# Kernel tuning notes

Measured on AMD Instinct MI355X. Metric: run time of the kernel, lower is better.

## Reference

```python
import jax, jax.numpy as jnp
import numpy as np

N_HEADS = 16


def _apply_rope(x, rope):
    # x: [B, H, N, Dh], rope: [B, N, Dh]; consecutive (even, odd) pairs form complex numbers
    xr, xi = x[..., 0::2], x[..., 1::2]              # [B,H,N,Dh/2]
    rr, ri = rope[:, None, :, 0::2], rope[:, None, :, 1::2]  # [B,1,N,Dh/2]
    or_ = xr * rr - xi * ri
    oi = xr * ri + xi * rr
    return jnp.stack([or_, oi], axis=-1).reshape(x.shape)


def setup_inputs() -> dict:
    key = jax.random.key(0)
    ks = jax.random.split(key, 8)
    B, N, D, Dh = 2, 2048, 2048, 128
    s = 0.02
    return {
        "x": jax.random.normal(ks[0], (B, N, D), jnp.float32),
        "q_rope": jax.random.normal(ks[1], (B, N, Dh), jnp.float32),
        "k_rope": jax.random.normal(ks[2], (B, N, Dh), jnp.float32),
        "Wq": jax.random.normal(ks[3], (D, D), jnp.float32) * s,
        "Wk": jax.random.normal(ks[4], (D, D), jnp.float32) * s,
        "Wv": jax.random.normal(ks[5], (D, D), jnp.float32) * s,
        "Wo": jax.random.normal(ks[6], (D, D), jnp.float32) * s,
        "bo": jax.random.normal(ks[7], (D,), jnp.float32) * s,
    }


def reference(x, q_rope, k_rope, Wq, Wk, Wv, Wo, bo):
    B, N, D = x.shape
    H = N_HEADS
    Dh = D // H
    # QKV projections (weights stored as [in, out])
    q = (x @ Wq).reshape(B, N, H, Dh).transpose(0, 2, 1, 3)  # [B,H,N,Dh]
    k = (x @ Wk).reshape(B, N, H, Dh).transpose(0, 2, 1, 3)
    v = (x @ Wv).reshape(B, N, H, Dh).transpose(0, 2, 1, 3)
    # NOTE: original scales q by d_head^-0.5 AND F.sdpa applies its default
    # 1/sqrt(d_head) scale again -> total score scale 1/d_head (faithful).
    q = q * (Dh ** -0.5)
    q = _apply_rope(q, q_rope)
    k = _apply_rope(k, k_rope)
    scores = jnp.einsum('bhnd,bhmd->bhnm', q, k) * (Dh ** -0.5)
    attn = jax.nn.softmax(scores, axis=-1)
    out = jnp.einsum('bhnm,bhmd->bhnd', attn, v)  # [B,H,N,Dh]
    out = out.transpose(0, 2, 1, 3).reshape(B, N, D)
    return out @ Wo + bo
```

## Files before the change

### kernel.cpp

```cpp
#include <hip/hip_runtime.h>
#include <hip/hip_bf16.h>
#include <stdint.h>


typedef __attribute__((ext_vector_type(4))) float f32x4;
typedef __attribute__((ext_vector_type(8))) short bf16x8;

__device__ __forceinline__ unsigned short f2bf(float f){
  unsigned u = __builtin_bit_cast(unsigned, f);
  u += 0x7FFFu + ((u >> 16) & 1u);
  return (unsigned short)(u >> 16);
}
__device__ __forceinline__ float bf2f(unsigned short h){
  unsigned u = ((unsigned)h) << 16;
  return __builtin_bit_cast(float, u);
}
__device__ __forceinline__ void gload16(const void* g, void* l){
  __builtin_amdgcn_global_load_lds((const __attribute__((address_space(1))) void*)g,
                                   (__attribute__((address_space(3))) void*)l, 16, 0, 0);
}
__device__ __forceinline__ void drain_all(){
  asm volatile("s_waitcnt vmcnt(0) lgkmcnt(0)" ::: "memory");
  __builtin_amdgcn_sched_barrier(0);
}

__global__ void k_cvt(const float* __restrict__ src, unsigned short* __restrict__ dst, int n4){
  int i = blockIdx.x * 256 + threadIdx.x;
  if (i >= n4) return;
  float4 v = ((const float4*)src)[i];
  unsigned long long pk = (unsigned long long)f2bf(v.x)
    | ((unsigned long long)f2bf(v.y) << 16)
    | ((unsigned long long)f2bf(v.z) << 32)
    | ((unsigned long long)f2bf(v.w) << 48);
  ((unsigned long long*)dst)[i] = pk;
}

__global__ void k_transpose_all(const float* __restrict__ W0, const float* __restrict__ W1,
                                const float* __restrict__ W2, const float* __restrict__ W3,
                                unsigned short* __restrict__ WT){
  const float* W = (blockIdx.z == 0) ? W0 : (blockIdx.z == 1) ? W1 : (blockIdx.z == 2) ? W2 : W3;
  unsigned short* dst = WT + (size_t)blockIdx.z * 4194304;
  __shared__ float tile[64][65];
  int t = threadIdx.x;
  int cc = t & 63, rb = t >> 6;
  int bx = blockIdx.x * 64;
  int by = blockIdx.y * 64;
  #pragma unroll
  for (int i = 0; i < 16; i++){
    int r = rb + i * 4;
    tile[r][cc] = W[(size_t)(by + r) * 2048 + bx + cc];
  }
  __syncthreads();
  #pragma unroll
  for (int i = 0; i < 16; i++){
    int r = rb + i * 4;
    dst[(size_t)(bx + r) * 2048 + by + cc] = f2bf(tile[cc][r]);
  }
}

__global__ __launch_bounds__(512, 2) void k_gemm_qkv(
    const unsigned short* __restrict__ A,
    const unsigned short* __restrict__ Bt,
    unsigned short* __restrict__ Oq,
    unsigned short* __restrict__ Ok,
    unsigned short* __restrict__ Ov,
    const float* __restrict__ ropeq,
    const float* __restrict__ ropek)
{
  const int Kdim = 2048;
  __shared__ char sh[98304];
  const int tid = threadIdx.x;
  const int w = tid >> 6, l = tid & 63, g = l >> 4, c = l & 15;
  const int i0 = blockIdx.y * 16 + blockIdx.x;
  const int xcd = i0 & 7, r0 = i0 >> 3;
  const int bm = (xcd * 2 + (r0 & 1)) * 256;
  const int bn = (r0 >> 1) * 128;
  const int mw = (w >> 1) * 64, nw = (w & 1) * 64;
  f32x4 acc[4][4] = {};
  const int srow = l >> 3;
  const int sbyte = (((l & 7) ^ srow) << 4);
  const char* Ab = (const char*)A;
  const char* Bb = (const char*)Bt;

  auto stage = [&](int kt, int buf){
    char* Abuf = sh + buf * 49152;
    char* Bbuf = Abuf + 32768;
    #pragma unroll
    for (int j = 0; j < 4; j++){
      int ch = w * 4 + j;
      int row = ch * 8 + srow;
      gload16(Ab + ((size_t)(bm + row) * Kdim + kt) * 2 + sbyte, Abuf + ch * 1024);
    }
    #pragma unroll
    for (int j = 0; j < 2; j++){
      int ch = w * 2 + j;
      int row = ch * 8 + srow;
      gload16(Bb + ((size_t)(bn + row) * Kdim + kt) * 2 + sbyte, Bbuf + ch * 1024);
    }
  };

  stage(0, 0);
  drain_all();
  __syncthreads();
  for (int t = 0; t < 32; t++){
    int cur = t & 1;
    if (t < 31) stage((t + 1) * 64, cur ^ 1);
    char* Abuf = sh + cur * 49152;
    char* Bbuf = Abuf + 32768;
    #pragma unroll
    for (int kk = 0; kk < 2; kk++){
      bf16x8 av[4], bv[4];
      #pragma unroll
      for (int i = 0; i < 4; i++){
        int m = mw + i * 16 + c;
        av[i] = *(const bf16x8*)(Abuf + m * 128 + ((kk * 64 + g * 16) ^ ((m & 7) << 4)));
        int n = nw + i * 16 + c;
        bv[i] = *(const bf16x8*)(Bbuf + n * 128 + ((kk * 64 + g * 16) ^ ((n & 7) << 4)));
      }
      #pragma unroll
      for (int i = 0; i < 4; i++)
        #pragma unroll
        for (int jj = 0; jj < 4; jj++)
          acc[i][jj] = __builtin_amdgcn_mfma_f32_16x16x32_bf16(av[i], bv[jj], acc[i][jj], 0, 0, 0);
    }
    drain_all();
    __syncthreads();
  }

  const int matsel = bn >> 11;
  const int hh = (bn >> 7) & 15;
  if (matsel < 2){
    unsigned short* O = matsel ? Ok : Oq;
    const float* rope = matsel ? ropek : ropeq;
    const float scale = matsel ? 1.0f : (1.0f / 128.0f);
    #pragma unroll
    for (int i = 0; i < 4; i++){
      int m0 = bm + mw + i * 16 + g * 4;
      #pragma unroll
      for (int jj = 0; jj < 4; jj++){
        int d = nw + jj * 16 + c;
        int dbase = d & ~1;
        int odd = d & 1;
        #pragma unroll
        for (int r = 0; r < 4; r++){
          int m = m0 + r;
          int b = m >> 11, tok = m & 2047;
          float v = acc[i][jj][r];
          float vp = __shfl_xor(v, 1);
          float2 rv = *(const float2*)(rope + (((size_t)(b * 2048 + tok)) << 7) + dbase);
          float xr = odd ? vp : v;
          float xi = odd ? v : vp;
          float res = odd ? (xr * rv.y + xi * rv.x) : (xr * rv.x - xi * rv.y);
          O[(((size_t)(b * 16 + hh) * 2048 + tok) << 7) + d] = f2bf(res * scale);
        }
      }
    }
  } else {
    #pragma unroll
    for (int i = 0; i < 4; i++){
      int m0 = bm + mw + i * 16 + g * 4;
      int b = m0 >> 11, tok0 = m0 & 2047;
      #pragma unroll
      for (int jj = 0; jj < 4; jj++){
        int d = nw + jj * 16 + c;
        unsigned long long pk = (unsigned long long)f2bf(acc[i][jj][0])
          | ((unsigned long long)f2bf(acc[i][jj][1]) << 16)
          | ((unsigned long long)f2bf(acc[i][jj][2]) << 32)
          | ((unsigned long long)f2bf(acc[i][jj][3]) << 48);
        *(unsigned long long*)(Ov + ((size_t)(b * 16 + hh) * 128 + d) * 2048 + tok0) = pk;
      }
    }
  }
}

__global__ __launch_bounds__(512, 2) void k_gemm_out(
    const unsigned short* __restrict__ A,
    const unsigned short* __restrict__ Bt,
    float* __restrict__ O,
    const float* __restrict__ bias)
{
  const int Kdim = 2048;
  __shared__ char sh[98304];
  const int tid = threadIdx.x;
  const int w = tid >> 6, l = tid & 63, g = l >> 4, c = l & 15;
  const int i0 = blockIdx.y * 16 + blockIdx.x;
  const int xcd = i0 & 7, r0 = i0 >> 3;
  const int bm = (xcd * 2 + (r0 & 1)) * 256;
  const int bn = (r0 >> 1) * 128;
  const int mw = (w >> 1) * 64, nw = (w & 1) * 64;
  f32x4 acc[4][4] = {};
  const int srow = l >> 3;
  const int sbyte = (((l & 7) ^ srow) << 4);
  const char* Ab = (const char*)A;
  const char* Bb = (const char*)Bt;

  auto stage = [&](int kt, int buf){
    char* Abuf = sh + buf * 49152;
    char* Bbuf = Abuf + 32768;
    #pragma unroll
    for (int j = 0; j < 4; j++){
      int ch = w * 4 + j;
      int row = ch * 8 + srow;
      gload16(Ab + ((size_t)(bm + row) * Kdim + kt) * 2 + sbyte, Abuf + ch * 1024);
    }
    #pragma unroll
    for (int j = 0; j < 2; j++){
      int ch = w * 2 + j;
      int row = ch * 8 + srow;
      gload16(Bb + ((size_t)(bn + row) * Kdim + kt) * 2 + sbyte, Bbuf + ch * 1024);
    }
  };

  stage(0, 0);
  drain_all();
  __syncthreads();
  for (int t = 0; t < 32; t++){
    int cur = t & 1;
    if (t < 31) stage((t + 1) * 64, cur ^ 1);
    char* Abuf = sh + cur * 49152;
    char* Bbuf = Abuf + 32768;
    #pragma unroll
    for (int kk = 0; kk < 2; kk++){
      bf16x8 av[4], bv[4];
      #pragma unroll
      for (int i = 0; i < 4; i++){
        int m = mw + i * 16 + c;
        av[i] = *(const bf16x8*)(Abuf + m * 128 + ((kk * 64 + g * 16) ^ ((m & 7) << 4)));
        int n = nw + i * 16 + c;
        bv[i] = *(const bf16x8*)(Bbuf + n * 128 + ((kk * 64 + g * 16) ^ ((n & 7) << 4)));
      }
      #pragma unroll
      for (int i = 0; i < 4; i++)
        #pragma unroll
        for (int jj = 0; jj < 4; jj++)
          acc[i][jj] = __builtin_amdgcn_mfma_f32_16x16x32_bf16(av[i], bv[jj], acc[i][jj], 0, 0, 0);
    }
    drain_all();
    __syncthreads();
  }
  #pragma unroll
  for (int i = 0; i < 4; i++){
    int m0 = bm + mw + i * 16 + g * 4;
    #pragma unroll
    for (int jj = 0; jj < 4; jj++){
      int n = bn + nw + jj * 16 + c;
      float bv2 = bias[n];
      #pragma unroll
      for (int r = 0; r < 4; r++)
        O[(size_t)(m0 + r) * 2048 + n] = acc[i][jj][r] + bv2;
    }
  }
}

__global__ __launch_bounds__(256, 2) void k_attn(
    const unsigned short* __restrict__ Q,
    const unsigned short* __restrict__ Kg,
    const unsigned short* __restrict__ VT,
    unsigned short* __restrict__ Ao)
{
  __shared__ char sh[81920];
  char* PsB = sh + 65536;
  const int tid = threadIdx.x;
  const int w = tid >> 6, l = tid & 63, g = l >> 4, c = l & 15;
  const int i0 = blockIdx.y * 16 + blockIdx.x;
  const int xcd = i0 & 7, kb2 = i0 >> 3;
  const int bh = xcd * 4 + (kb2 >> 4);
  const int qt = kb2 & 15;
  const char* Qb = (const char*)(Q + (((size_t)bh * 2048 + qt * 128) << 7));
  const char* Kb = (const char*)(Kg + ((size_t)bh << 18));
  const char* Vb = (const char*)(VT + ((size_t)bh << 18));
  const int rsub = l >> 4;
  const int byte0 = (l & 15) << 4;
  const int drow = l >> 3;
  const int vbyte = (((l & 7) ^ drow) << 4);

  #pragma unroll
  for (int j = 0; j < 8; j++){
    int chunk = w * 8 + j;
    int row = chunk * 4 + rsub;
    gload16(Qb + (size_t)row * 256 + (byte0 ^ ((row & 7) << 4)), sh + chunk * 1024);
  }
  __syncthreads();
  bf16x8 qa[4][2];
  #pragma unroll
  for (int kk = 0; kk < 4; kk++)
    #pragma unroll
    for (int mf = 0; mf < 2; mf++){
      int q = w * 32 + mf * 16 + c;
      qa[kk][mf] = *(const bf16x8*)(sh + q * 256 + ((kk * 64 + g * 16) ^ ((q & 7) << 4)));
    }
  __syncthreads();

  auto stageKV = [&](int kv, int buf){
    char* Kc = sh + buf * 16384;
    char* Vc = sh + 32768 + buf * 16384;
    #pragma unroll
    for (int j = 0; j < 4; j++){
      int chunk = w * 4 + j;
      int row = chunk * 4 + rsub;
      gload16(Kb + (size_t)(kv * 64 + row) * 256 + (byte0 ^ ((row & 7) << 4)), Kc + chunk * 1024);
    }
    #pragma unroll
    for (int j = 0; j < 4; j++){
      int chunk = w * 4 + j;
      int d = chunk * 8 + drow;
      gload16(Vb + (size_t)d * 4096 + kv * 128 + vbyte, Vc + chunk * 1024);
    }
  };

  f32x4 oacc[2][8] = {};
  float lpart[2][4] = {};

  stageKV(0, 0);
  __syncthreads();

  for (int kv = 0; kv < 32; kv++){
    int cur = kv & 1;
    if (kv < 31) stageKV(kv + 1, cur ^ 1);
    char* Kc = sh + cur * 16384;
    char* Vc = sh + 32768 + cur * 16384;

    f32x4 sacc[2][4] = {};
    __builtin_amdgcn_s_setprio(1);
    #pragma unroll
    for (int kk = 0; kk < 4; kk++){
      bf16x8 kbf[4];
      #pragma unroll
      for (int nf = 0; nf < 4; nf++){
        int kx = nf * 16 + c;
        kbf[nf] = *(const bf16x8*)(Kc + kx * 256 + ((kk * 64 + g * 16) ^ ((kx & 7) << 4)));
      }
      #pragma unroll
      for (int mf = 0; mf < 2; mf++)
        #pragma unroll
        for (int nf = 0; nf < 4; nf++)
          sacc[mf][nf] = __builtin_amdgcn_mfma_f32_16x16x32_bf16(qa[kk][mf], kbf[nf], sacc[mf][nf], 0, 0, 0);
    }
    __builtin_amdgcn_s_setprio(0);

    #pragma unroll
    for (int mf = 0; mf < 2; mf++)
      #pragma unroll
      for (int nf = 0; nf < 4; nf++)
        #pragma unroll
        for (int r = 0; r < 4; r++){
          float pv = __expf(sacc[mf][nf][r]);
          sacc[mf][nf][r] = pv;
          lpart[mf][r] += pv;
        }

    #pragma unroll
    for (int mf = 0; mf < 2; mf++)
      #pragma unroll
      for (int nf = 0; nf < 4; nf++)
        #pragma unroll
        for (int r = 0; r < 4; r++){
          int q = w * 32 + mf * 16 + g * 4 + r;
          int key = nf * 16 + c;
          *(unsigned short*)(PsB + q * 128 + ((key * 2) ^ (((q >> 2) & 3) << 5))) = f2bf(sacc[mf][nf][r]);
        }
    asm volatile("s_waitcnt lgkmcnt(0)" ::: "memory");
    __builtin_amdgcn_sched_barrier(0);

    __builtin_amdgcn_s_setprio(1);
    #pragma unroll
    for (int kk = 0; kk < 2; kk++){
      bf16x8 pa[2], vv[8];
      #pragma unroll
      for (int mf = 0; mf < 2; mf++){
        int q = w * 32 + mf * 16 + c;
        pa[mf] = *(const bf16x8*)(PsB + q * 128 + ((kk * 64 + g * 16) ^ (((q >> 2) & 3) << 5)));
      }
      #pragma unroll
      for (int df = 0; df < 8; df++){
        int d = df * 16 + c;
        vv[df] = *(const bf16x8*)(Vc + d * 128 + ((kk * 64 + g * 16) ^ ((d & 7) << 4)));
      }
      #pragma unroll
      for (int mf = 0; mf < 2; mf++)
        #pragma unroll
        for (int df = 0; df < 8; df++)
          oacc[mf][df] = __builtin_amdgcn_mfma_f32_16x16x32_bf16(pa[mf], vv[df], oacc[mf][df], 0, 0, 0);
    }
    __builtin_amdgcn_s_setprio(0);
    drain_all();
    __syncthreads();
  }

  int b = bh >> 4, h = bh & 15;
  #pragma unroll
  for (int mf = 0; mf < 2; mf++)
    #pragma unroll
    for (int r = 0; r < 4; r++){
      float s = lpart[mf][r];
      #pragma unroll
      for (int off = 1; off < 16; off <<= 1) s += __shfl_xor(s, off);
      float inv = 1.f / s;
      int qg = qt * 128 + w * 32 + mf * 16 + g * 4 + r;
      size_t rowbase = ((size_t)(b * 2048 + qg)) * 2048 + h * 128;
      #pragma unroll
      for (int df = 0; df < 8; df++)
        Ao[rowbase + df * 16 + c] = f2bf(oacc[mf][df][r] * inv);
    }
}

extern "C" void kernel_launch(void* const* d_in, const int* in_sizes, int n_in,
                              void* d_out, int out_size, void* d_ws, size_t ws_size,
                              hipStream_t stream){
  const float* x      = (const float*)d_in[0];
  const float* q_rope = (const float*)d_in[1];
  const float* k_rope = (const float*)d_in[2];
  const float* Wq     = (const float*)d_in[3];
  const float* Wk     = (const float*)d_in[4];
  const float* Wv     = (const float*)d_in[5];
  const float* Wo     = (const float*)d_in[6];
  const float* bo     = (const float*)d_in[7];
  char* ws = (char*)d_ws;
  unsigned short* xb  = (unsigned short*)(ws);
  unsigned short* wqT = (unsigned short*)(ws + 16777216);
  unsigned short* woT = (unsigned short*)(ws + 41943040);
  unsigned short* qb  = (unsigned short*)(ws + 50331648);
  unsigned short* kbf = (unsigned short*)(ws + 67108864);
  unsigned short* vt  = (unsigned short*)(ws + 83886080);
  unsigned short* ab  = (unsigned short*)(ws + 100663296);

  k_cvt<<<8192, 256, 0, stream>>>(x, xb, 2097152);
  dim3 tg(32, 32, 4);
  k_transpose_all<<<tg, 256, 0, stream>>>(Wq, Wk, Wv, Wo, wqT);
  dim3 gq(16, 48);
  k_gemm_qkv<<<gq, 512, 0, stream>>>(xb, wqT, qb, kbf, vt, q_rope, k_rope);
  dim3 ga(16, 32);
  k_attn<<<ga, 256, 0, stream>>>(qb, kbf, vt, ab);
  dim3 go(16, 16);
  k_gemm_out<<<go, 512, 0, stream>>>(ab, woT, (float*)d_out, bo);
}
```

Baseline: 255.9 us.

## Shrink QKV GEMM tile to 128x128 with 256 threads and single-buffered LDS

The QKV projection GEMM moves from 256x128 block tiles with 512 threads and a double-buffered 96 KB LDS pipeline to 128x128 tiles with 256 threads and a single 32 KB staging buffer. Each k-step now loads, synchronizes, then computes, and the grid doubles in the M direction. The aim is more resident blocks per CU and more blocks for better load balance. In exchange, global loads no longer overlap with MFMA work inside a block, and A-tile reuse per block is lower.

New measurement: 263.7 us. +3.0%, slower.

```diff
diff --git a/kernel.cpp b/kernel.cpp
--- a/kernel.cpp
+++ b/kernel.cpp
@@ -58,7 +58,7 @@
   }
 }
 
-__global__ __launch_bounds__(512, 2) void k_gemm_qkv(
+__global__ __launch_bounds__(256, 3) void k_gemm_qkv(
     const unsigned short* __restrict__ A,
     const unsigned short* __restrict__ Bt,
     unsigned short* __restrict__ Oq,
@@ -68,54 +68,41 @@
     const float* __restrict__ ropek)
 {
   const int Kdim = 2048;
-  __shared__ char sh[98304];
+  __shared__ unsigned short As[128 * 64];
+  __shared__ unsigned short Bs[128 * 64];
   const int tid = threadIdx.x;
   const int w = tid >> 6, l = tid & 63, g = l >> 4, c = l & 15;
-  const int i0 = blockIdx.y * 16 + blockIdx.x;
+  const int i0 = blockIdx.y * 32 + blockIdx.x;
   const int xcd = i0 & 7, r0 = i0 >> 3;
-  const int bm = (xcd * 2 + (r0 & 1)) * 256;
-  const int bn = (r0 >> 1) * 128;
+  const int bm = (xcd * 4 + (r0 & 3)) * 128;
+  const int bn = (r0 >> 2) * 128;
   const int mw = (w >> 1) * 64, nw = (w & 1) * 64;
   f32x4 acc[4][4] = {};
   const int srow = l >> 3;
   const int sbyte = (((l & 7) ^ srow) << 4);
   const char* Ab = (const char*)A;
   const char* Bb = (const char*)Bt;
-
-  auto stage = [&](int kt, int buf){
-    char* Abuf = sh + buf * 49152;
-    char* Bbuf = Abuf + 32768;
+  char* AsB = (char*)As; char* BsB = (char*)Bs;
+
+  for (int kt = 0; kt < Kdim; kt += 64){
+    __syncthreads();
     #pragma unroll
     for (int j = 0; j < 4; j++){
-      int ch = w * 4 + j;
-      int row = ch * 8 + srow;
-      gload16(Ab + ((size_t)(bm + row) * Kdim + kt) * 2 + sbyte, Abuf + ch * 1024);
-    }
-    #pragma unroll
-    for (int j = 0; j < 2; j++){
-      int ch = w * 2 + j;
-      int row = ch * 8 + srow;
-      gload16(Bb + ((size_t)(bn + row) * Kdim + kt) * 2 + sbyte, Bbuf + ch * 1024);
-    }
-  };
-
-  stage(0, 0);
-  drain_all();
-  __syncthreads();
-  for (int t = 0; t < 32; t++){
-    int cur = t & 1;
-    if (t < 31) stage((t + 1) * 64, cur ^ 1);
-    char* Abuf = sh + cur * 49152;
-    char* Bbuf = Abuf + 32768;
+      int chunk = w * 4 + j;
+      int row = chunk * 8 + srow;
+      gload16(Ab + ((size_t)(bm + row) * Kdim + kt) * 2 + sbyte, AsB + chunk * 1024);
+      gload16(Bb + ((size_t)(bn + row) * Kdim + kt) * 2 + sbyte, BsB + chunk * 1024);
+    }
+    __syncthreads();
     #pragma unroll
     for (int kk = 0; kk < 2; kk++){
       bf16x8 av[4], bv[4];
       #pragma unroll
       for (int i = 0; i < 4; i++){
         int m = mw + i * 16 + c;
-        av[i] = *(const bf16x8*)(Abuf + m * 128 + ((kk * 64 + g * 16) ^ ((m & 7) << 4)));
+        av[i] = *(const bf16x8*)(AsB + m * 128 + ((kk * 64 + g * 16) ^ ((m & 7) << 4)));
         int n = nw + i * 16 + c;
-        bv[i] = *(const bf16x8*)(Bbuf + n * 128 + ((kk * 64 + g * 16) ^ ((n & 7) << 4)));
+        bv[i] = *(const bf16x8*)(BsB + n * 128 + ((kk * 64 + g * 16) ^ ((n & 7) << 4)));
       }
       #pragma unroll
       for (int i = 0; i < 4; i++)
@@ -123,8 +110,6 @@
         for (int jj = 0; jj < 4; jj++)
           acc[i][jj] = __builtin_amdgcn_mfma_f32_16x16x32_bf16(av[i], bv[jj], acc[i][jj], 0, 0, 0);
     }
-    drain_all();
-    __syncthreads();
   }
 
   const int matsel = bn >> 11;
@@ -427,8 +412,8 @@
   k_cvt<<<8192, 256, 0, stream>>>(x, xb, 2097152);
   dim3 tg(32, 32, 4);
   k_transpose_all<<<tg, 256, 0, stream>>>(Wq, Wk, Wv, Wo, wqT);
-  dim3 gq(16, 48);
-  k_gemm_qkv<<<gq, 512, 0, stream>>>(xb, wqT, qb, kbf, vt, q_rope, k_rope);
+  dim3 gq(32, 48);
+  k_gemm_qkv<<<gq, 256, 0, stream>>>(xb, wqT, qb, kbf, vt, q_rope, k_rope);
   dim3 ga(16, 32);
   k_attn<<<ga, 256, 0, stream>>>(qb, kbf, vt, ab);
   dim3 go(16, 16);
```
